# Kernel tuning notes

Measured on AMD Instinct MI355X. Metric: run time of the kernel, lower is better.

The kernel has to match this reference:

```python
import jax, jax.numpy as jnp
import numpy as np

EMBED_DIM = 1024
NUM_HEADS = 16
HEAD_DIM = EMBED_DIM // NUM_HEADS


def setup_inputs() -> dict:
    key = jax.random.key(0)
    ks = jax.random.split(key, 5)
    scale = 1.0 / np.sqrt(EMBED_DIM)
    x = jax.random.normal(ks[0], (2, 2048, EMBED_DIM), dtype=jnp.float32)
    W_qkv = jax.random.uniform(ks[1], (EMBED_DIM, 3 * EMBED_DIM), jnp.float32, -scale, scale)
    b_qkv = jax.random.uniform(ks[2], (3 * EMBED_DIM,), jnp.float32, -scale, scale)
    W_out = jax.random.uniform(ks[3], (EMBED_DIM, EMBED_DIM), jnp.float32, -scale, scale)
    b_out = jax.random.uniform(ks[4], (EMBED_DIM,), jnp.float32, -scale, scale)
    return {"x": x, "W_qkv": W_qkv, "b_qkv": b_qkv, "W_out": W_out, "b_out": b_out}


def reference(x, W_qkv, b_qkv, W_out, b_out):
    B, T, C = x.shape
    H, D = NUM_HEADS, HEAD_DIM
    qkv = x @ W_qkv + b_qkv                       # [B,T,3C]
    q, k, v = jnp.split(qkv, 3, axis=-1)
    # [B,T,C] -> [B,H,T,D]
    q = q.reshape(B, T, H, D).transpose(0, 2, 1, 3)
    k = k.reshape(B, T, H, D).transpose(0, 2, 1, 3)
    v = v.reshape(B, T, H, D).transpose(0, 2, 1, 3)
    scores = jnp.einsum('bhqd,bhkd->bhqk', q, k) / np.sqrt(D)
    attn = jax.nn.softmax(scores, axis=-1)
    out = jnp.einsum('bhqk,bhkd->bhqd', attn, v)  # [B,H,T,D]
    out = out.transpose(0, 2, 1, 3).reshape(B, T, C)
    return out @ W_out + b_out
```

## Files before the change

kernel.cpp:

```cpp
#include <hip/hip_runtime.h>
#include <hip/hip_bf16.h>

#define TB 2048
#define CC 1024
#define HH 16
#define DD 64
#define MM 4096
#define N3 3072
#define KVB 128
#define NT (TB / KVB)

typedef __bf16 bf16x8 __attribute__((ext_vector_type(8)));
typedef float f32x4 __attribute__((ext_vector_type(4)));
typedef unsigned short ushort8 __attribute__((ext_vector_type(8)));
typedef unsigned short u16;

#define QSCALE 0.180336880693612f

__device__ __forceinline__ u16 f2b(float f) {
    unsigned int x = __float_as_uint(f);
    x = (x + 0x7fffu + ((x >> 16) & 1u)) >> 16;
    return (u16)x;
}

__device__ __forceinline__ unsigned cvt_pk_bf16(float lo, float hi) {
    unsigned r;
    asm("v_cvt_pk_bf16_f32 %0, %1, %2" : "=v"(r) : "v"(lo), "v"(hi));
    return r;
}

__device__ __forceinline__ void gld16(const u16* g, u16* l) {
    __builtin_amdgcn_global_load_lds(
        (const __attribute__((address_space(1))) unsigned int*)g,
        (__attribute__((address_space(3))) unsigned int*)l, 16, 0, 0);
}

__global__ __launch_bounds__(256) void prep(const float* __restrict__ x,
                                            u16* __restrict__ xb,
                                            const float* __restrict__ wqkv,
                                            u16* __restrict__ wqkvT,
                                            const float* __restrict__ wout,
                                            u16* __restrict__ woutT) {
    __shared__ float tl[64][65];
    const int bx = blockIdx.x;
    const int tid = threadIdx.x;
    if (bx < 4096) {
        int i = (bx * 256 + tid) * 4;
        float4 v = *reinterpret_cast<const float4*>(x + i);
        union { u16 u[4]; uint2 v2; } r;
        r.u[0] = f2b(v.x); r.u[1] = f2b(v.y); r.u[2] = f2b(v.z); r.u[3] = f2b(v.w);
        *reinterpret_cast<uint2*>(xb + i) = r.v2;
        return;
    }
    const int idx = bx - 4096;
    const int nb = idx & 63, kb = idx >> 6;
    const float* in; u16* out; int N, n0;
    if (nb < 48) { in = wqkv; out = wqkvT; N = 3072; n0 = nb * 64; }
    else         { in = wout; out = woutT; N = 1024; n0 = (nb - 48) * 64; }
    const int k0 = kb * 64;
#pragma unroll
    for (int rep = 0; rep < 16; ++rep) {
        int id2 = rep * 256 + tid;
        int r = id2 >> 6, c = id2 & 63;
        tl[r][c] = in[(size_t)(k0 + r) * N + n0 + c];
    }
    __syncthreads();
#pragma unroll
    for (int rep = 0; rep < 16; ++rep) {
        int id2 = rep * 256 + tid;
        int r = id2 >> 6, c = id2 & 63;
        out[(size_t)(n0 + r) * 1024 + k0 + c] = f2b(tl[c][r]);
    }
}

__global__ __launch_bounds__(256) void gemm_qkv(const u16* __restrict__ xb,
                                                const u16* __restrict__ wT,
                                                const float* __restrict__ bias,
                                                u16* __restrict__ qg,
                                                u16* __restrict__ kg,
                                                u16* __restrict__ vtg) {
    __shared__ u16 smem[2 * 128 * 64];
    u16* As = smem;
    u16* Bs = smem + 128 * 64;
    const int m0 = blockIdx.y * 128, n0 = blockIdx.x * 128;
    const int tid = threadIdx.x;
    const int w = tid >> 6, lane = tid & 63, lr = lane & 15, h = lane >> 4;
    const int wr = w >> 1, wc = w & 1;
    f32x4 acc[4][4] = {};

    for (int k0 = 0; k0 < 1024; k0 += 64) {
        __syncthreads();
#pragma unroll
        for (int j = 0; j < 4; ++j) {
            int L = j * 256 + tid;
            int r = L >> 3, c = L & 7;
            int csw = (c ^ (r & 7)) << 3;
            gld16(xb + (size_t)(m0 + r) * 1024 + k0 + csw, As + L * 8);
            gld16(wT + (size_t)(n0 + r) * 1024 + k0 + csw, Bs + L * 8);
        }
        __syncthreads();
#pragma unroll
        for (int kk = 0; kk < 2; ++kk) {
            bf16x8 a[4], b[4];
            int cc = kk * 4 + h;
#pragma unroll
            for (int m = 0; m < 4; ++m) {
                int R = wr * 64 + m * 16 + lr;
                a[m] = *reinterpret_cast<const bf16x8*>((const char*)As + R * 128 + ((cc ^ (R & 7)) << 4));
            }
#pragma unroll
            for (int n = 0; n < 4; ++n) {
                int R = wc * 64 + n * 16 + lr;
                b[n] = *reinterpret_cast<const bf16x8*>((const char*)Bs + R * 128 + ((cc ^ (R & 7)) << 4));
            }
#pragma unroll
            for (int m = 0; m < 4; ++m)
#pragma unroll
                for (int n = 0; n < 4; ++n)
                    acc[m][n] = __builtin_amdgcn_mfma_f32_16x16x32_bf16(a[m], b[n], acc[m][n], 0, 0, 0);
        }
    }

    const int nthird = n0 >> 10;
    if (nthird == 2) {
        __syncthreads();
#pragma unroll
        for (int n = 0; n < 4; ++n) {
            int nloc = wc * 64 + n * 16 + lr;
            unsigned xorv = (unsigned)(nloc & 15) << 4;
            float bv = bias[n0 + nloc];
#pragma unroll
            for (int m = 0; m < 4; ++m) {
                int mloc = wr * 64 + m * 16 + h * 4;
                int mp = (mloc & ~31) | (((mloc >> 2) & 3) << 3) | (((mloc >> 4) & 1) << 2);
                union { u16 u[4]; unsigned long long ll; } pk4;
#pragma unroll
                for (int reg = 0; reg < 4; ++reg)
                    pk4.u[reg] = f2b(acc[m][n][reg] + bv);
                *reinterpret_cast<unsigned long long*>(
                    (char*)smem + nloc * 256 + ((unsigned)(mp * 2) ^ xorv)) = pk4.ll;
            }
        }
        __syncthreads();
        const int b = m0 >> 11, t0 = m0 & 2047;
        const int c16 = tid & 15;
#pragma unroll
        for (int step = 0; step < 8; ++step) {
            int row = (tid >> 4) + step * 16;
            ushort8 vch = *reinterpret_cast<const ushort8*>(
                (const char*)smem + row * 256 + ((unsigned)((c16 ^ (row & 15)) << 4)));
            int c1 = (n0 + row) & 1023;
            int hh = c1 >> 6, dd = c1 & 63;
            *reinterpret_cast<ushort8*>(
                vtg + ((size_t)(b * HH + hh) * DD + dd) * TB + t0 + c16 * 8) = vch;
        }
    } else {
#pragma unroll
        for (int n = 0; n < 4; ++n) {
            int ng = n0 + wc * 64 + n * 16 + lr;
            int c1 = ng & 1023;
            int hh = c1 >> 6, dd = c1 & 63;
            float bv = bias[ng];
#pragma unroll
            for (int m = 0; m < 4; ++m) {
#pragma unroll
                for (int reg = 0; reg < 4; ++reg) {
                    int mg = m0 + wr * 64 + m * 16 + h * 4 + reg;
                    int b = mg >> 11, t = mg & 2047;
                    size_t bh = (size_t)b * HH + hh;
                    float val = acc[m][n][reg] + bv;
                    if (nthird == 0) qg[(bh * TB + t) * DD + dd] = f2b(val * QSCALE);
                    else             kg[(bh * TB + t) * DD + dd] = f2b(val);
                }
            }
        }
    }
}

__global__ __launch_bounds__(512, 4) void attn(const u16* __restrict__ qg,
                                               const u16* __restrict__ kg,
                                               const u16* __restrict__ vtg,
                                               u16* __restrict__ ao) {
    __shared__ u16 Kt[2][KVB * 64];
    __shared__ u16 Vt[2][64 * KVB];
    const int bh = blockIdx.y;
    const int q0 = blockIdx.x * 128;
    const int tid = threadIdx.x, w = tid >> 6, lane = tid & 63;
    const int lr = lane & 15, h = lane >> 4;
    const u16* qb = qg + (size_t)bh * TB * DD;
    const u16* kb = kg + (size_t)bh * TB * DD;
    const u16* vb = vtg + (size_t)bh * DD * TB;

#define STAGE(buf, kp, vp) do {                                                         \
    _Pragma("unroll")                                                                   \
    for (int j = 0; j < 2; ++j) {                                                       \
        int L = j * 512 + tid;                                                          \
        int rk = L >> 3, ck = L & 7;                                                    \
        gld16((kp) + (size_t)rk * DD + ((ck ^ (rk & 7)) << 3), Kt[buf] + L * 8);        \
        int rv = L >> 4, cv = L & 15;                                                   \
        gld16((vp) + (size_t)rv * TB + ((cv ^ (rv & 15)) << 3), Vt[buf] + L * 8);       \
    } } while (0)

    bf16x8 bq[2];
#pragma unroll
    for (int kk = 0; kk < 2; ++kk)
        bq[kk] = *reinterpret_cast<const bf16x8*>(qb + (size_t)(q0 + w * 16 + lr) * DD + kk * 32 + h * 8);

    f32x4 o[4] = {};
    float m_r = -1e30f;
    float l_r = 0.f;
    const f32x4 zero4 = {0.f, 0.f, 0.f, 0.f};

    auto tile_body = [&](const u16* ktc, const u16* vtc) {
        f32x4 s[8];
        __builtin_amdgcn_s_setprio(1);
        {
            int cc0 = h;
#pragma unroll
            for (int ng = 0; ng < 8; ++ng) {
                int R = ng * 16 + lr;
                bf16x8 ak = *reinterpret_cast<const bf16x8*>((const char*)ktc + R * 128 + ((cc0 ^ (R & 7)) << 4));
                s[ng] = __builtin_amdgcn_mfma_f32_16x16x32_bf16(ak, bq[0], zero4, 0, 0, 0);
            }
            int cc1 = 4 + h;
#pragma unroll
            for (int ng = 0; ng < 8; ++ng) {
                int R = ng * 16 + lr;
                bf16x8 ak = *reinterpret_cast<const bf16x8*>((const char*)ktc + R * 128 + ((cc1 ^ (R & 7)) << 4));
                s[ng] = __builtin_amdgcn_mfma_f32_16x16x32_bf16(ak, bq[1], s[ng], 0, 0, 0);
            }
        }
        __builtin_amdgcn_s_setprio(0);

        float tmx[8];
#pragma unroll
        for (int ng = 0; ng < 8; ++ng)
            tmx[ng] = fmaxf(fmaxf(s[ng][0], s[ng][1]), fmaxf(s[ng][2], s[ng][3]));
        float pm = fmaxf(fmaxf(fmaxf(tmx[0], tmx[1]), fmaxf(tmx[2], tmx[3])),
                         fmaxf(fmaxf(tmx[4], tmx[5]), fmaxf(tmx[6], tmx[7])));
        pm = fmaxf(pm, __shfl_xor(pm, 16));
        pm = fmaxf(pm, __shfl_xor(pm, 32));

        if (!__all(pm - m_r <= 8.0f)) {
            float mn = fmaxf(m_r, pm);
            float fr = __builtin_amdgcn_exp2f(m_r - mn);
            m_r = mn;
            l_r *= fr;
#pragma unroll
            for (int reg = 0; reg < 4; ++reg) {
                float fro = __shfl(fr, h * 4 + reg);
#pragma unroll
                for (int ngd = 0; ngd < 4; ++ngd)
                    o[ngd][reg] *= fro;
            }
        }

        float ps[8];
#pragma unroll
        for (int ng = 0; ng < 8; ++ng) {
            s[ng][0] = __builtin_amdgcn_exp2f(s[ng][0] - m_r);
            s[ng][1] = __builtin_amdgcn_exp2f(s[ng][1] - m_r);
            s[ng][2] = __builtin_amdgcn_exp2f(s[ng][2] - m_r);
            s[ng][3] = __builtin_amdgcn_exp2f(s[ng][3] - m_r);
            ps[ng] = (s[ng][0] + s[ng][1]) + (s[ng][2] + s[ng][3]);
        }
        float sum = ((ps[0] + ps[1]) + (ps[2] + ps[3])) + ((ps[4] + ps[5]) + (ps[6] + ps[7]));
        sum += __shfl_xor(sum, 16);
        sum += __shfl_xor(sum, 32);
        l_r += sum;

        __builtin_amdgcn_s_setprio(1);
#pragma unroll
        for (int kk = 0; kk < 4; ++kk) {
            union { unsigned u[4]; bf16x8 v; } ap;
            ap.u[0] = cvt_pk_bf16(s[2 * kk][0], s[2 * kk][1]);
            ap.u[1] = cvt_pk_bf16(s[2 * kk][2], s[2 * kk][3]);
            ap.u[2] = cvt_pk_bf16(s[2 * kk + 1][0], s[2 * kk + 1][1]);
            ap.u[3] = cvt_pk_bf16(s[2 * kk + 1][2], s[2 * kk + 1][3]);
            int cpos = kk * 4 + h;
#pragma unroll
            for (int ngd = 0; ngd < 4; ++ngd) {
                int d = ngd * 16 + lr;
                bf16x8 bv = *reinterpret_cast<const bf16x8*>((const char*)vtc + d * 256 + ((cpos ^ (d & 15)) << 4));
                o[ngd] = __builtin_amdgcn_mfma_f32_16x16x32_bf16(ap.v, bv, o[ngd], 0, 0, 0);
            }
        }
        __builtin_amdgcn_s_setprio(0);
    };

    STAGE(0, kb, vb);
    const u16* kp = kb + KVB * DD;
    const u16* vp = vb + KVB;
    __syncthreads();

#pragma unroll 1
    for (int kt2 = 0; kt2 < NT / 2; ++kt2) {
        STAGE(1, kp, vp);
        kp += KVB * DD; vp += KVB;
        tile_body(Kt[0], Vt[0]);
        __syncthreads();
        if (kt2 < NT / 2 - 1) {
            STAGE(0, kp, vp);
            kp += KVB * DD; vp += KVB;
        }
        tile_body(Kt[1], Vt[1]);
        __syncthreads();
    }
#undef STAGE

    float linv[4];
#pragma unroll
    for (int reg = 0; reg < 4; ++reg)
        linv[reg] = 1.0f / __shfl(l_r, h * 4 + reg);

    const int b = bh >> 4, hh = bh & 15;
#pragma unroll
    for (int ngd = 0; ngd < 4; ++ngd) {
#pragma unroll
        for (int reg = 0; reg < 4; ++reg) {
            int t = q0 + w * 16 + h * 4 + reg;
            int col = hh * DD + ngd * 16 + lr;
            ao[((size_t)(b * TB + t)) * CC + col] = f2b(o[ngd][reg] * linv[reg]);
        }
    }
}

__global__ __launch_bounds__(256) void gemm_out(const u16* __restrict__ ao,
                                                const u16* __restrict__ wT,
                                                const float* __restrict__ bias,
                                                float* __restrict__ out) {
    __shared__ u16 As[64 * 64];
    __shared__ u16 Bs[128 * 64];
    const int m0 = blockIdx.y * 64, n0 = blockIdx.x * 128;
    const int tid = threadIdx.x;
    const int w = tid >> 6, lane = tid & 63, lr = lane & 15, h = lane >> 4;
    f32x4 acc[4][2] = {};

    for (int k0 = 0; k0 < 1024; k0 += 64) {
        __syncthreads();
#pragma unroll
        for (int j = 0; j < 2; ++j) {
            int L = j * 256 + tid;
            int r = L >> 3, c = L & 7;
            gld16(ao + (size_t)(m0 + r) * 1024 + k0 + ((c ^ (r & 7)) << 3), As + L * 8);
        }
#pragma unroll
        for (int j = 0; j < 4; ++j) {
            int L = j * 256 + tid;
            int r = L >> 3, c = L & 7;
            gld16(wT + (size_t)(n0 + r) * 1024 + k0 + ((c ^ (r & 7)) << 3), Bs + L * 8);
        }
        __syncthreads();
#pragma unroll
        for (int kk = 0; kk < 2; ++kk) {
            bf16x8 a[4], b[2];
            int cc = kk * 4 + h;
#pragma unroll
            for (int m = 0; m < 4; ++m) {
                int R = m * 16 + lr;
                a[m] = *reinterpret_cast<const bf16x8*>((const char*)As + R * 128 + ((cc ^ (R & 7)) << 4));
            }
#pragma unroll
            for (int n = 0; n < 2; ++n) {
                int R = w * 32 + n * 16 + lr;
                b[n] = *reinterpret_cast<const bf16x8*>((const char*)Bs + R * 128 + ((cc ^ (R & 7)) << 4));
            }
#pragma unroll
            for (int m = 0; m < 4; ++m)
#pragma unroll
                for (int n = 0; n < 2; ++n)
                    acc[m][n] = __builtin_amdgcn_mfma_f32_16x16x32_bf16(a[m], b[n], acc[m][n], 0, 0, 0);
        }
    }

#pragma unroll
    for (int n = 0; n < 2; ++n) {
        int ng = n0 + w * 32 + n * 16 + lr;
        float bv = bias[ng];
#pragma unroll
        for (int m = 0; m < 4; ++m) {
#pragma unroll
            for (int reg = 0; reg < 4; ++reg) {
                int mg = m0 + m * 16 + h * 4 + reg;
                out[(size_t)mg * 1024 + ng] = acc[m][n][reg] + bv;
            }
        }
    }
}

extern "C" void kernel_launch(void* const* d_in, const int* in_sizes, int n_in,
                              void* d_out, int out_size, void* d_ws, size_t ws_size,
                              hipStream_t stream) {
    const float* x     = (const float*)d_in[0];
    const float* W_qkv = (const float*)d_in[1];
    const float* b_qkv = (const float*)d_in[2];
    const float* W_out = (const float*)d_in[3];
    const float* b_out = (const float*)d_in[4];
    float* out = (float*)d_out;

    char* ws = (char*)d_ws;
    u16* xb    = (u16*)(ws);
    u16* wqkvT = (u16*)(ws + (size_t)( 8u << 20));
    u16* woutT = (u16*)(ws + (size_t)(14u << 20));
    u16* qg    = (u16*)(ws + (size_t)(16u << 20));
    u16* kg    = (u16*)(ws + (size_t)(24u << 20));
    u16* vtg   = (u16*)(ws + (size_t)(32u << 20));
    u16* ao    = xb;

    hipLaunchKernelGGL(prep, dim3(5120), dim3(256), 0, stream, x, xb, W_qkv, wqkvT, W_out, woutT);
    hipLaunchKernelGGL(gemm_qkv, dim3(24, 32), dim3(256), 0, stream, xb, wqkvT, b_qkv, qg, kg, vtg);
    hipLaunchKernelGGL(attn, dim3(16, 32), dim3(512), 0, stream, qg, kg, vtg, ao);
    hipLaunchKernelGGL(gemm_out, dim3(8, 64), dim3(256), 0, stream, ao, woutT, b_out, out);
}
```

Baseline: 121.5 us.

## Stage Q/K epilogue through LDS for vectorized stores; swap attention grid order

The Q and K outputs of the QKV GEMM epilogue were written as scattered 2-byte global stores. They are now packed into a swizzled shared-memory tile and written back as 16-byte vector stores along the head dimension. Separately, the attention grid is transposed so consecutive blocks cover different heads instead of different query tiles of the same head, which changes L2 reuse of K/V. The staging adds two barriers and extra LDS traffic in the epilogue.

```diff
diff --git a/kernel.cpp b/kernel.cpp
--- a/kernel.cpp
+++ b/kernel.cpp
@@ -122,6 +122,7 @@
     }
 
     const int nthird = n0 >> 10;
+    const int b = m0 >> 11, t0 = m0 & 2047;
     if (nthird == 2) {
         __syncthreads();
 #pragma unroll
@@ -142,7 +143,6 @@
             }
         }
         __syncthreads();
-        const int b = m0 >> 11, t0 = m0 & 2047;
         const int c16 = tid & 15;
 #pragma unroll
         for (int step = 0; step < 8; ++step) {
@@ -155,24 +155,36 @@
                 vtg + ((size_t)(b * HH + hh) * DD + dd) * TB + t0 + c16 * 8) = vch;
         }
     } else {
+        const float qs = (nthird == 0) ? QSCALE : 1.0f;
+        __syncthreads();
 #pragma unroll
         for (int n = 0; n < 4; ++n) {
-            int ng = n0 + wc * 64 + n * 16 + lr;
-            int c1 = ng & 1023;
+            int nloc = wc * 64 + n * 16 + lr;
+            float bv = bias[n0 + nloc];
+#pragma unroll
+            for (int m = 0; m < 4; ++m) {
+#pragma unroll
+                for (int reg = 0; reg < 4; ++reg) {
+                    int mloc = wr * 64 + m * 16 + h * 4 + reg;
+                    *reinterpret_cast<u16*>((char*)smem + mloc * 256 +
+                        ((unsigned)(nloc * 2) ^ ((unsigned)(mloc & 15) << 4)))
+                        = f2b((acc[m][n][reg] + bv) * qs);
+                }
+            }
+        }
+        __syncthreads();
+        u16* dst = (nthird == 0) ? qg : kg;
+        const int c16 = tid & 15;
+#pragma unroll
+        for (int step = 0; step < 8; ++step) {
+            int row = (tid >> 4) + step * 16;
+            ushort8 vch = *reinterpret_cast<const ushort8*>(
+                (const char*)smem + row * 256 + ((unsigned)((c16 ^ (row & 15)) << 4)));
+            int colbase = c16 * 8;
+            int c1 = (n0 + colbase) & 1023;
             int hh = c1 >> 6, dd = c1 & 63;
-            float bv = bias[ng];
-#pragma unroll
-            for (int m = 0; m < 4; ++m) {
-#pragma unroll
-                for (int reg = 0; reg < 4; ++reg) {
-                    int mg = m0 + wr * 64 + m * 16 + h * 4 + reg;
-                    int b = mg >> 11, t = mg & 2047;
-                    size_t bh = (size_t)b * HH + hh;
-                    float val = acc[m][n][reg] + bv;
-                    if (nthird == 0) qg[(bh * TB + t) * DD + dd] = f2b(val * QSCALE);
-                    else             kg[(bh * TB + t) * DD + dd] = f2b(val);
-                }
-            }
+            *reinterpret_cast<ushort8*>(
+                dst + ((size_t)(b * HH + hh) * TB + (t0 + row)) * DD + dd) = vch;
         }
     }
 }
@@ -183,8 +195,8 @@
                                                u16* __restrict__ ao) {
     __shared__ u16 Kt[2][KVB * 64];
     __shared__ u16 Vt[2][64 * KVB];
-    const int bh = blockIdx.y;
-    const int q0 = blockIdx.x * 128;
+    const int bh = blockIdx.x;
+    const int q0 = blockIdx.y * 128;
     const int tid = threadIdx.x, w = tid >> 6, lane = tid & 63;
     const int lr = lane & 15, h = lane >> 4;
     const u16* qb = qg + (size_t)bh * TB * DD;
@@ -409,6 +421,6 @@
 
     hipLaunchKernelGGL(prep, dim3(5120), dim3(256), 0, stream, x, xb, W_qkv, wqkvT, W_out, woutT);
     hipLaunchKernelGGL(gemm_qkv, dim3(24, 32), dim3(256), 0, stream, xb, wqkvT, b_qkv, qg, kg, vtg);
-    hipLaunchKernelGGL(attn, dim3(16, 32), dim3(512), 0, stream, qg, kg, vtg, ao);
+    hipLaunchKernelGGL(attn, dim3(32, 16), dim3(512), 0, stream, qg, kg, vtg, ao);
     hipLaunchKernelGGL(gemm_out, dim3(8, 64), dim3(256), 0, stream, ao, woutT, b_out, out);
 }
```

Result: faster. 118.4 us (-2.5%).
